# Kernel tuning notes

Hardware: AMD Instinct MI355X
Metric: run time of the kernel (lower is better)

Reference implementation:

```python
import jax, jax.numpy as jnp
import numpy as np

B, S, D, H, DFF = 4, 2048, 1024, 16, 4096
HD = D // H  # head_dim = 64


def rmsnorm(x, scale, eps=1e-6):
    var = jnp.mean(jnp.square(x), axis=-1, keepdims=True)
    return x * jax.lax.rsqrt(var + eps) * scale


def setup_inputs() -> dict:
    key = jax.random.key(0)
    ks = jax.random.split(key, 16)
    s = 1.0 / np.sqrt(D)
    inp = {
        "x": jax.random.normal(ks[0], (B, S, D), jnp.float32),
        "wq": jax.random.normal(ks[1], (D, D), jnp.float32) * s,
        "bq": jnp.zeros((D,), jnp.float32),
        "wk": jax.random.normal(ks[2], (D, D), jnp.float32) * s,
        "bk": jnp.zeros((D,), jnp.float32),
        "wv": jax.random.normal(ks[3], (D, D), jnp.float32) * s,
        "bv": jnp.zeros((D,), jnp.float32),
        "wbeta": jax.random.normal(ks[4], (D, H), jnp.float32) * s,
        "bbeta": jnp.zeros((H,), jnp.float32),
        "wo": jax.random.normal(ks[5], (D, D), jnp.float32) * s,
        "bo": jnp.zeros((D,), jnp.float32),
        "w1": jax.random.normal(ks[6], (D, DFF), jnp.float32) * s,
        "b1": jnp.zeros((DFF,), jnp.float32),
        "w2": jax.random.normal(ks[7], (DFF, D), jnp.float32) * (1.0 / np.sqrt(DFF)),
        "b2": jnp.zeros((D,), jnp.float32),
        "ln1_scale": jnp.ones((D,), jnp.float32),
        "ln2_scale": jnp.ones((D,), jnp.float32),
    }
    return inp


def gdn_attention(x, wq, bq, wk, bk, wv, bv, wbeta, bbeta, wo, bo):
    b, s, _ = x.shape
    q = (x @ wq + bq).reshape(b, s, H, HD)
    k = (x @ wk + bk).reshape(b, s, H, HD)
    v = (x @ wv + bv).reshape(b, s, H, HD)
    k = k / (jnp.linalg.norm(k, axis=-1, keepdims=True) + 1e-6)
    beta = jax.nn.sigmoid(x @ wbeta + bbeta)[..., None]  # (b, s, H, 1)

    # time-major for scan: (s, b, H, ...)
    q = jnp.transpose(q, (1, 0, 2, 3))
    k = jnp.transpose(k, (1, 0, 2, 3))
    v = jnp.transpose(v, (1, 0, 2, 3))
    beta = jnp.transpose(beta, (1, 0, 2, 3))

    def _step(Sm, inputs):
        q_t, k_t, v_t, beta_t = inputs
        Sk = jnp.einsum('bhde,bhe->bhd', Sm, k_t)
        delta = v_t - Sk
        Sm = Sm + beta_t[..., None] * jnp.einsum('bhd,bhe->bhde', delta, k_t)
        o_t = jnp.einsum('bhde,bhe->bhd', Sm, q_t)
        return Sm, o_t

    S0 = jnp.zeros((b, H, HD, HD), x.dtype)
    _, outputs = jax.lax.scan(_step, S0, (q, k, v, beta))
    outputs = jnp.transpose(outputs, (1, 0, 2, 3)).reshape(b, s, D)
    return outputs @ wo + bo


def reference(x, wq, bq, wk, bk, wv, bv, wbeta, bbeta, wo, bo,
              w1, b1, w2, b2, ln1_scale, ln2_scale):
    residual = x
    h = rmsnorm(x, ln1_scale)
    h = gdn_attention(h, wq, bq, wk, bk, wv, bv, wbeta, bbeta, wo, bo)
    x = h + residual
    residual = x
    h = rmsnorm(x, ln2_scale)
    h = jax.nn.gelu(h @ w1 + b1) @ w2 + b2
    return h + residual
```

## Files before the change

kernel.cpp:

```cpp
#include <hip/hip_runtime.h>

#define DEV __device__ __forceinline__

typedef short bf16x8 __attribute__((ext_vector_type(8)));
typedef float f32x4 __attribute__((ext_vector_type(4)));
typedef unsigned int uint;

#define SBAR()   asm volatile("s_barrier" ::: "memory")
#define WAITV(n) asm volatile("s_waitcnt vmcnt(" #n ")" ::: "memory")
#define WAITL()  asm volatile("s_waitcnt lgkmcnt(0)" ::: "memory")

DEV unsigned short f2b(float f) {
    uint u = __float_as_uint(f);
    u += 0x7fffu + ((u >> 16) & 1u);
    return (unsigned short)(u >> 16);
}
DEV uint packbf2(float a, float b) { return (uint)f2b(a) | ((uint)f2b(b) << 16); }
DEV float b2f(unsigned short s) { return __uint_as_float(((uint)s) << 16); }
DEV float b2f_lo(uint u) { return __uint_as_float(u << 16); }
DEV float b2f_hi(uint u) { return __uint_as_float(u & 0xffff0000u); }

DEV void async_cp16(const void* g, void* l) {
    __builtin_amdgcn_global_load_lds(
        (const __attribute__((address_space(1))) unsigned int*)g,
        (__attribute__((address_space(3))) unsigned int*)l, 16, 0, 0);
}

DEV float quad_sum(float x) {
    x += __int_as_float(__builtin_amdgcn_update_dpp(0, __float_as_int(x), 0xB1, 0xF, 0xF, true));
    x += __int_as_float(__builtin_amdgcn_update_dpp(0, __float_as_int(x), 0x4E, 0xF, 0xF, true));
    return x;
}

DEV float gelu_f(float u) {
    float p = u + 0.044715f * u * u * u;
    float e = __expf(-1.5957691216f * p);
    return __fdividef(u, 1.f + e);
}

DEV void dec8(uint4 p, float* o) {
    o[0] = b2f_lo(p.x); o[1] = b2f_hi(p.x); o[2] = b2f_lo(p.y); o[3] = b2f_hi(p.y);
    o[4] = b2f_lo(p.z); o[5] = b2f_hi(p.z); o[6] = b2f_lo(p.w); o[7] = b2f_hi(p.w);
}

__global__ __launch_bounds__(256) void transpose_cast_k(
    const float* __restrict__ in, unsigned short* __restrict__ out, int K, int N)
{
    __shared__ float tile[32][33];
    const int k0 = blockIdx.x * 32, n0 = blockIdx.y * 32;
    const int tx = threadIdx.x & 31, ty = threadIdx.x >> 5;
#pragma unroll
    for (int i = 0; i < 32; i += 8) {
        int n = n0 + tx;
        tile[ty + i][tx] = (n < N) ? in[(size_t)(k0 + ty + i) * N + n] : 0.0f;
    }
    __syncthreads();
#pragma unroll
    for (int i = 0; i < 32; i += 8) {
        out[(size_t)(n0 + ty + i) * K + (k0 + tx)] = f2b(tile[tx][ty + i]);
    }
}

__global__ void build_bias_k(const float* __restrict__ bq, const float* __restrict__ bk,
                             const float* __restrict__ bv, const float* __restrict__ bb,
                             float* __restrict__ outb)
{
    int i = blockIdx.x * 256 + threadIdx.x;
    if (i >= 3328) return;
    float v = 0.f;
    if (i < 1024)      v = bq[i];
    else if (i < 2048) v = bk[i - 1024];
    else if (i < 3072) v = bv[i - 2048];
    else if (i < 3088) v = bb[i - 3072];
    outb[i] = v;
}

__global__ __launch_bounds__(256) void rmsnorm_cast_k(
    const float* __restrict__ x, const float* __restrict__ scale,
    unsigned short* __restrict__ out)
{
    const int row = blockIdx.x;
    const int t = threadIdx.x;
    const float4 v = *(const float4*)(x + (size_t)row * 1024 + t * 4);
    float ss = v.x * v.x + v.y * v.y + v.z * v.z + v.w * v.w;
#pragma unroll
    for (int off = 1; off < 64; off <<= 1) ss += __shfl_xor(ss, off);
    __shared__ float wsum[4];
    if ((t & 63) == 0) wsum[t >> 6] = ss;
    __syncthreads();
    const float tot = wsum[0] + wsum[1] + wsum[2] + wsum[3];
    const float inv = rsqrtf(tot * (1.0f / 1024.0f) + 1e-6f);
    const float4 sc = *(const float4*)(scale + t * 4);
    uint lo = (uint)f2b(v.x * inv * sc.x) | ((uint)f2b(v.y * inv * sc.y) << 16);
    uint hi = (uint)f2b(v.z * inv * sc.z) | ((uint)f2b(v.w * inv * sc.w) << 16);
    uint2 pkd; pkd.x = lo; pkd.y = hi;
    *(uint2*)(out + (size_t)row * 1024 + t * 4) = pkd;
}

template <bool GELU, bool GUARD>
__global__ __launch_bounds__(512, 2) void gemm256(
    const unsigned short* __restrict__ A, const unsigned short* __restrict__ BT,
    const float* __restrict__ bias, unsigned short* __restrict__ C,
    int Nstride, int Nreal, int K)
{
    __shared__ __align__(16) unsigned short As[4][256 * 32];
    __shared__ __align__(16) unsigned short Bs[4][256 * 32];
    const int tid = threadIdx.x;
    const int wid = tid >> 6;
    const int lane = tid & 63;
    const int l16 = lane & 15, quad = lane >> 4;
    const int wm = wid & 1, wn = wid >> 1;
    const int m0 = blockIdx.x << 8, n0 = blockIdx.y << 8;

    const int srow = (wid << 5) + (lane >> 2);
    const int scol = ((lane & 3) ^ ((lane >> 3) & 3)) << 3;
    const unsigned short* Ag = A + (size_t)(m0 + srow) * K + scol;
    const unsigned short* Bg = BT + (size_t)(n0 + srow) * K + scol;
    const size_t rstep16 = (size_t)16 * K;
    const int ldst = wid << 10;

    f32x4 acc[8][4];
#pragma unroll
    for (int i = 0; i < 8; i++)
#pragma unroll
        for (int j = 0; j < 4; j++) acc[i][j] = (f32x4)0.f;

    const int ksw = (quad ^ ((l16 >> 1) & 3)) << 3;
    const int aoff = ((wm << 7) + l16) * 32 + ksw;
    const int boff = ((wn << 6) + l16) * 32 + ksw;

    const int nt = K >> 5;
    async_cp16(Ag, &As[0][ldst]);
    async_cp16(Ag + rstep16, &As[0][ldst + 512]);
    async_cp16(Bg, &Bs[0][ldst]);
    async_cp16(Bg + rstep16, &Bs[0][ldst + 512]);
    async_cp16(Ag + 32, &As[1][ldst]);
    async_cp16(Ag + 32 + rstep16, &As[1][ldst + 512]);
    async_cp16(Bg + 32, &Bs[1][ldst]);
    async_cp16(Bg + 32 + rstep16, &Bs[1][ldst + 512]);
    WAITV(4);
    SBAR();

    for (int tb = 0; tb < nt; tb += 4) {
#pragma unroll
        for (int u = 0; u < 4; ++u) {
            const int t = tb + u;
            const int pb = (u + 2) & 3;
            const bool st = (t + 2) < nt;
            const size_t kpre = (size_t)(t + 2) << 5;
            bf16x8 af[4], bfr[4];
#pragma unroll
            for (int mi = 0; mi < 4; mi++) af[mi] = *(const bf16x8*)&As[u][aoff + mi * 512];
#pragma unroll
            for (int ni = 0; ni < 4; ni++) bfr[ni] = *(const bf16x8*)&Bs[u][boff + ni * 512];
            if (st) {
                async_cp16(Ag + kpre, &As[pb][ldst]);
                async_cp16(Ag + kpre + rstep16, &As[pb][ldst + 512]);
            }
            SBAR();
            WAITL();
            __builtin_amdgcn_s_setprio(1);
#pragma unroll
            for (int mi = 0; mi < 4; mi++)
#pragma unroll
                for (int ni = 0; ni < 4; ni++)
                    acc[mi][ni] = __builtin_amdgcn_mfma_f32_16x16x32_bf16(af[mi], bfr[ni], acc[mi][ni], 0, 0, 0);
            __builtin_amdgcn_s_setprio(0);
            SBAR();
#pragma unroll
            for (int mi = 0; mi < 4; mi++) af[mi] = *(const bf16x8*)&As[u][aoff + (mi + 4) * 512];
            if (st) {
                async_cp16(Bg + kpre, &Bs[pb][ldst]);
                async_cp16(Bg + kpre + rstep16, &Bs[pb][ldst + 512]);
                WAITV(4);
            } else {
                WAITV(0);
            }
            SBAR();
            WAITL();
            __builtin_amdgcn_s_setprio(1);
#pragma unroll
            for (int mi = 0; mi < 4; mi++)
#pragma unroll
                for (int ni = 0; ni < 4; ni++)
                    acc[mi + 4][ni] = __builtin_amdgcn_mfma_f32_16x16x32_bf16(af[mi], bfr[ni], acc[mi + 4][ni], 0, 0, 0);
            __builtin_amdgcn_s_setprio(0);
            SBAR();
        }
    }

    float bv[4];
    const int ccol = n0 + (wn << 6) + l16;
#pragma unroll
    for (int ni = 0; ni < 4; ni++) bv[ni] = bias[ccol + ni * 16];
#pragma unroll
    for (int mi = 0; mi < 8; mi++) {
        const int row = m0 + (wm << 7) + mi * 16 + (quad << 2);
#pragma unroll
        for (int r = 0; r < 4; r++) {
            unsigned short* Crow = C + (size_t)(row + r) * Nstride + ccol;
#pragma unroll
            for (int ni = 0; ni < 4; ni++) {
                float v = acc[mi][ni][r] + bv[ni];
                if (GELU) v = gelu_f(v);
                if (!GUARD || (ccol + ni * 16) < Nreal) Crow[ni * 16] = f2b(v);
            }
        }
    }
}

template <bool ADD>
__global__ __launch_bounds__(512, 2) void gemm128n256(
    const unsigned short* __restrict__ A, const unsigned short* __restrict__ BT,
    const float* __restrict__ bias, const float* __restrict__ add,
    float* __restrict__ C, int N, int K)
{
    __shared__ __align__(16) unsigned short As[4][128 * 32];
    __shared__ __align__(16) unsigned short Bs[4][256 * 32];
    const int tid = threadIdx.x;
    const int wid = tid >> 6;
    const int lane = tid & 63;
    const int l16 = lane & 15, quad = lane >> 4;
    const int wm = wid & 1, wn = wid >> 1;
    const int m0 = blockIdx.x << 7, n0 = blockIdx.y << 8;

    const int arow = (wid << 4) + (lane >> 2);
    const int brow = (wid << 5) + (lane >> 2);
    const int scol = ((lane & 3) ^ ((lane >> 3) & 3)) << 3;
    const unsigned short* Ag = A + (size_t)(m0 + arow) * K + scol;
    const unsigned short* Bg = BT + (size_t)(n0 + brow) * K + scol;
    const size_t rstep16 = (size_t)16 * K;
    const int lda = wid << 9;
    const int ldb = wid << 10;

    f32x4 acc[4][4];
#pragma unroll
    for (int i = 0; i < 4; i++)
#pragma unroll
        for (int j = 0; j < 4; j++) acc[i][j] = (f32x4)0.f;

    const int ksw = (quad ^ ((l16 >> 1) & 3)) << 3;
    const int aoff = ((wm << 6) + l16) * 32 + ksw;
    const int boff = ((wn << 6) + l16) * 32 + ksw;

    const int nt = K >> 5;
    async_cp16(Ag, &As[0][lda]);
    async_cp16(Bg, &Bs[0][ldb]);
    async_cp16(Bg + rstep16, &Bs[0][ldb + 512]);
    async_cp16(Ag + 32, &As[1][lda]);
    async_cp16(Bg + 32, &Bs[1][ldb]);
    async_cp16(Bg + 32 + rstep16, &Bs[1][ldb + 512]);
    WAITV(3);
    SBAR();

    for (int tb = 0; tb < nt; tb += 4) {
#pragma unroll
        for (int u = 0; u < 4; ++u) {
            const int t = tb + u;
            const int pb = (u + 2) & 3;
            const bool st = (t + 2) < nt;
            const size_t kpre = (size_t)(t + 2) << 5;
            bf16x8 af[4], bfr[4];
#pragma unroll
            for (int mi = 0; mi < 4; mi++) af[mi] = *(const bf16x8*)&As[u][aoff + mi * 512];
#pragma unroll
            for (int ni = 0; ni < 4; ni++) bfr[ni] = *(const bf16x8*)&Bs[u][boff + ni * 512];
            if (st) {
                async_cp16(Ag + kpre, &As[pb][lda]);
                async_cp16(Bg + kpre, &Bs[pb][ldb]);
                async_cp16(Bg + kpre + rstep16, &Bs[pb][ldb + 512]);
            }
            SBAR();
            WAITL();
            __builtin_amdgcn_s_setprio(1);
#pragma unroll
            for (int mi = 0; mi < 4; mi++)
#pragma unroll
                for (int ni = 0; ni < 4; ni++)
                    acc[mi][ni] = __builtin_amdgcn_mfma_f32_16x16x32_bf16(af[mi], bfr[ni], acc[mi][ni], 0, 0, 0);
            __builtin_amdgcn_s_setprio(0);
            if (st) { WAITV(3); } else { WAITV(0); }
            SBAR();
        }
    }

    const int ccol = n0 + (wn << 6) + l16;
    float bv[4];
#pragma unroll
    for (int ni = 0; ni < 4; ni++) bv[ni] = bias[ccol + ni * 16];
#pragma unroll
    for (int mi = 0; mi < 4; mi++) {
        const int row = m0 + (wm << 6) + mi * 16 + (quad << 2);
#pragma unroll
        for (int r = 0; r < 4; r++) {
#pragma unroll
            for (int ni = 0; ni < 4; ni++) {
                size_t idx = (size_t)(row + r) * N + ccol + ni * 16;
                float v = acc[mi][ni][r] + bv[ni];
                if (ADD) v += add[idx];
                C[idx] = v;
            }
        }
    }
}


__global__ __launch_bounds__(256) void gdn_prep(
    unsigned short* __restrict__ qkv, unsigned short* __restrict__ Wg,
    unsigned short* __restrict__ ZTg, unsigned short* __restrict__ KTg)
{
    const int chunk = blockIdx.x, bh = blockIdx.y;
    const int b = bh >> 4, h = bh & 15;
    __shared__ float Ks[64 * 68];
    __shared__ float Ws[64 * 65];
    __shared__ float Zs[64 * 65];
    __shared__ float Asl[64 * 65];
    __shared__ float bs[64];
    const int tid = threadIdx.x;
    const int t = tid >> 2, c = tid & 3;
    unsigned short* rowp = qkv + (size_t)(b * 2048 + chunk * 64 + t) * 3200;

    float kn[16];
    {
        uint4 ka = *(const uint4*)(rowp + 1024 + h * 64 + 16 * c);
        uint4 kb = *(const uint4*)(rowp + 1024 + h * 64 + 16 * c + 8);
        dec8(ka, kn); dec8(kb, kn + 8);
    }
    float ss = 0.f;
#pragma unroll
    for (int j = 0; j < 16; j++) ss += kn[j] * kn[j];
    ss = quad_sum(ss);
    const float inv = 1.f / (sqrtf(ss) + 1e-6f);
#pragma unroll
    for (int j = 0; j < 16; j++) kn[j] *= inv;
#pragma unroll
    for (int j = 0; j < 16; j++) Ks[t * 68 + 16 * c + j] = kn[j];
    {
        uint4 p0, p1;
        p0.x = packbf2(kn[0], kn[1]);  p0.y = packbf2(kn[2], kn[3]);
        p0.z = packbf2(kn[4], kn[5]);  p0.w = packbf2(kn[6], kn[7]);
        p1.x = packbf2(kn[8], kn[9]);  p1.y = packbf2(kn[10], kn[11]);
        p1.z = packbf2(kn[12], kn[13]); p1.w = packbf2(kn[14], kn[15]);
        *(uint4*)(rowp + 1024 + h * 64 + 16 * c) = p0;
        *(uint4*)(rowp + 1024 + h * 64 + 16 * c + 8) = p1;
    }
    if (c == 0) bs[t] = 1.f / (1.f + __expf(-b2f(rowp[3072 + h])));
    __syncthreads();

    const float beta = bs[t];
#pragma unroll
    for (int j = 0; j < 16; j++) Ws[t * 65 + 16 * c + j] = beta * kn[j];
    {
        float vv[16];
        uint4 va = *(const uint4*)(rowp + 2048 + h * 64 + 16 * c);
        uint4 vb = *(const uint4*)(rowp + 2048 + h * 64 + 16 * c + 8);
        dec8(va, vv); dec8(vb, vv + 8);
#pragma unroll
        for (int j = 0; j < 16; j++) Zs[t * 65 + 16 * c + j] = beta * vv[j];
    }
    __syncthreads();

    {
        const int tt = tid >> 4, sx = tid & 15;
        float dm[4][4];
#pragma unroll
        for (int i = 0; i < 4; i++)
#pragma unroll
            for (int j = 0; j < 4; j++) dm[i][j] = 0.f;
        for (int d = 0; d < 64; d++) {
            float kt[4], ksv[4];
#pragma unroll
            for (int i = 0; i < 4; i++) kt[i] = Ks[(4 * tt + i) * 68 + d];
#pragma unroll
            for (int j = 0; j < 4; j++) ksv[j] = Ks[(4 * sx + j) * 68 + d];
#pragma unroll
            for (int i = 0; i < 4; i++)
#pragma unroll
                for (int j = 0; j < 4; j++) dm[i][j] += kt[i] * ksv[j];
        }
#pragma unroll
        for (int i = 0; i < 4; i++)
#pragma unroll
            for (int j = 0; j < 4; j++) {
                int T = 4 * tt + i, S_ = 4 * sx + j;
                Asl[T * 65 + S_] = (S_ < T) ? bs[T] * dm[i][j] : 0.f;
            }
    }
    __syncthreads();

    {
        const int wid = tid >> 6, lane = tid & 63;
        for (int qi = 0; qi < 4; qi++) {
            if (qi > 0) {
                const int tb = qi * 16 + wid * 4;
                float aw[4], az[4];
#pragma unroll
                for (int i = 0; i < 4; i++) { aw[i] = Ws[(tb + i) * 65 + lane]; az[i] = Zs[(tb + i) * 65 + lane]; }
                for (int s = 0; s < qi * 16; s++) {
                    float wsv = Ws[s * 65 + lane], zsv = Zs[s * 65 + lane];
#pragma unroll
                    for (int i = 0; i < 4; i++) {
                        float a = Asl[(tb + i) * 65 + s];
                        aw[i] -= a * wsv; az[i] -= a * zsv;
                    }
                }
#pragma unroll
                for (int i = 0; i < 4; i++) { Ws[(tb + i) * 65 + lane] = aw[i]; Zs[(tb + i) * 65 + lane] = az[i]; }
            }
            __syncthreads();
            if (wid == 0) {
                for (int T = qi * 16; T < qi * 16 + 16; T++) {
                    float a_ = Ws[T * 65 + lane];
                    for (int s = qi * 16; s < T; s++) a_ -= Asl[T * 65 + s] * Ws[s * 65 + lane];
                    Ws[T * 65 + lane] = a_;
                }
            } else if (wid == 1) {
                for (int T = qi * 16; T < qi * 16 + 16; T++) {
                    float a_ = Zs[T * 65 + lane];
                    for (int s = qi * 16; s < T; s++) a_ -= Asl[T * 65 + s] * Zs[s * 65 + lane];
                    Zs[T * 65 + lane] = a_;
                }
            }
            __syncthreads();
        }
    }

    const size_t cbase = ((size_t)bh * 32 + chunk) * 4096;
    {
#pragma unroll
        for (int half = 0; half < 2; half++) {
            uint4 w4;
            w4.x = packbf2(Ws[t * 65 + 16 * c + half * 8 + 0], Ws[t * 65 + 16 * c + half * 8 + 1]);
            w4.y = packbf2(Ws[t * 65 + 16 * c + half * 8 + 2], Ws[t * 65 + 16 * c + half * 8 + 3]);
            w4.z = packbf2(Ws[t * 65 + 16 * c + half * 8 + 4], Ws[t * 65 + 16 * c + half * 8 + 5]);
            w4.w = packbf2(Ws[t * 65 + 16 * c + half * 8 + 6], Ws[t * 65 + 16 * c + half * 8 + 7]);
            *(uint4*)(Wg + cbase + (size_t)((2 * c + half) * 64 + t) * 8) = w4;
        }
    }
    {
        const int jj = tid >> 2, tq = tid & 3;
#pragma unroll
        for (int half = 0; half < 2; half++) {
            uint4 z4;
            int i0 = half * 8;
            z4.x = packbf2(Zs[(16 * tq + i0 + 0) * 65 + jj], Zs[(16 * tq + i0 + 1) * 65 + jj]);
            z4.y = packbf2(Zs[(16 * tq + i0 + 2) * 65 + jj], Zs[(16 * tq + i0 + 3) * 65 + jj]);
            z4.z = packbf2(Zs[(16 * tq + i0 + 4) * 65 + jj], Zs[(16 * tq + i0 + 5) * 65 + jj]);
            z4.w = packbf2(Zs[(16 * tq + i0 + 6) * 65 + jj], Zs[(16 * tq + i0 + 7) * 65 + jj]);
            *(uint4*)(ZTg + cbase + (size_t)((2 * tq + half) * 64 + jj) * 8) = z4;
        }
    }
    {
        const int dd = tid >> 2, tq = tid & 3;
#pragma unroll
        for (int half = 0; half < 2; half++) {
            uint4 k4;
            int i0 = half * 8;
            k4.x = packbf2(Ks[(16 * tq + i0 + 0) * 68 + dd], Ks[(16 * tq + i0 + 1) * 68 + dd]);
            k4.y = packbf2(Ks[(16 * tq + i0 + 2) * 68 + dd], Ks[(16 * tq + i0 + 3) * 68 + dd]);
            k4.z = packbf2(Ks[(16 * tq + i0 + 4) * 68 + dd], Ks[(16 * tq + i0 + 5) * 68 + dd]);
            k4.w = packbf2(Ks[(16 * tq + i0 + 6) * 68 + dd], Ks[(16 * tq + i0 + 7) * 68 + dd]);
            *(uint4*)(KTg + cbase + (size_t)((2 * tq + half) * 64 + dd) * 8) = k4;
        }
    }
}

__global__ __launch_bounds__(256, 1) void gdn_prop_mfma(
    const unsigned short* __restrict__ Wg, const unsigned short* __restrict__ KTg,
    const unsigned short* __restrict__ ZTg, unsigned short* __restrict__ Sg,
    unsigned short* __restrict__ YTg)
{
    const int bh = blockIdx.x;
    __shared__ unsigned short WbU[4096];
    __shared__ unsigned short KTbU[4096];
    __shared__ unsigned short ZTbU[4096];
    __shared__ unsigned short SbU[4096];
    const int tid = threadIdx.x;
    const int wid = tid >> 6;
    const int lane = tid & 63;
    const int l16 = lane & 15, quad = lane >> 4;

    f32x4 Sacc[4];
#pragma unroll
    for (int dt = 0; dt < 4; dt++) Sacc[dt] = (f32x4)0.f;

    for (int ch = 0; ch < 32; ch++) {
        const size_t cbase = ((size_t)bh * 32 + ch) * 4096;
#pragma unroll
        for (int p = 0; p < 2; p++) {
            const int n = wid * 2 + p;
            async_cp16(Wg + cbase + n * 512 + lane * 8, &WbU[n * 512]);
            async_cp16(KTg + cbase + n * 512 + lane * 8, &KTbU[n * 512]);
            async_cp16(ZTg + cbase + n * 512 + lane * 8, &ZTbU[n * 512]);
        }
#pragma unroll
        for (int dt = 0; dt < 4; dt++) {
#pragma unroll
            for (int r = 0; r < 4; r++) {
                const int j = wid * 16 + quad * 4 + r;
                SbU[((2 * dt + (l16 >> 3)) * 64 + j) * 8 + (l16 & 7)] = f2b(Sacc[dt][r]);
            }
        }
        __syncthreads();

        {
            uint4 sa0 = *(const uint4*)&SbU[tid * 16];
            uint4 sa1 = *(const uint4*)&SbU[tid * 16 + 8];
            *(uint4*)(Sg + cbase + tid * 16) = sa0;
            *(uint4*)(Sg + cbase + tid * 16 + 8) = sa1;
        }

        f32x4 t1[4];
#pragma unroll
        for (int tt = 0; tt < 4; tt++) t1[tt] = (f32x4)0.f;
#pragma unroll
        for (int kh = 0; kh < 2; kh++) {
            const int g = kh * 4 + quad;
            bf16x8 afr = *(const bf16x8*)&SbU[(g * 64 + wid * 16 + l16) * 8];
#pragma unroll
            for (int tt = 0; tt < 4; tt++) {
                bf16x8 bfr = *(const bf16x8*)&WbU[(g * 64 + tt * 16 + l16) * 8];
                t1[tt] = __builtin_amdgcn_mfma_f32_16x16x32_bf16(afr, bfr, t1[tt], 0, 0, 0);
            }
        }
#pragma unroll
        for (int tt = 0; tt < 4; tt++) {
            const int t = tt * 16 + l16;
            const int gb = (t >> 3) * 64;
            unsigned short ybf[4];
#pragma unroll
            for (int r = 0; r < 4; r++) {
                const int j = wid * 16 + quad * 4 + r;
                const float z = b2f(ZTbU[(gb + j) * 8 + (t & 7)]);
                ybf[r] = f2b(z - t1[tt][r]);
            }
#pragma unroll
            for (int r = 0; r < 4; r++) {
                const int j = wid * 16 + quad * 4 + r;
                ZTbU[(gb + j) * 8 + (t & 7)] = ybf[r];
            }
        }
#pragma unroll
        for (int kh = 0; kh < 2; kh++) {
            const int g = kh * 4 + quad;
            bf16x8 afr = *(const bf16x8*)&ZTbU[(g * 64 + wid * 16 + l16) * 8];
#pragma unroll
            for (int dt = 0; dt < 4; dt++) {
                bf16x8 bfr = *(const bf16x8*)&KTbU[(g * 64 + dt * 16 + l16) * 8];
                Sacc[dt] = __builtin_amdgcn_mfma_f32_16x16x32_bf16(afr, bfr, Sacc[dt], 0, 0, 0);
            }
        }
#pragma unroll
        for (int pp = 0; pp < 2; pp++) {
            const int p = lane * 2 + pp;
            const int g = p >> 4, jj = p & 15;
            const int off = (g * 64 + wid * 16 + jj) * 8;
            uint4 yv = *(const uint4*)&ZTbU[off];
            *(uint4*)(YTg + cbase + off) = yv;
        }
        __syncthreads();
    }
}

__global__ __launch_bounds__(256) void gdn_out(
    const unsigned short* __restrict__ qkv, const unsigned short* __restrict__ YTg,
    const unsigned short* __restrict__ Sg, unsigned short* __restrict__ attn)
{
    const int chunk = blockIdx.x, bh = blockIdx.y;
    const int b = bh >> 4, h = bh & 15;
    __shared__ unsigned short QbU[8 * 516];
    __shared__ unsigned short KbU[8 * 516];
    __shared__ unsigned short StU[8 * 516];
    __shared__ unsigned short YtU[8 * 516];
    __shared__ unsigned short MhU[8 * 516];
    __shared__ unsigned short MlU[8 * 516];
    const int tid = threadIdx.x;
    const int wid = tid >> 6, lane = tid & 63;
    const int l16 = lane & 15, quad = lane >> 4;
    const size_t cbase = ((size_t)bh * 32 + chunk) * 4096;

    {
        const int t = tid >> 2, c = tid & 3;
        const unsigned short* rowp = qkv + (size_t)(b * 2048 + chunk * 64 + t) * 3200;
        uint4 qa = *(const uint4*)(rowp + h * 64 + 16 * c);
        uint4 qb = *(const uint4*)(rowp + h * 64 + 16 * c + 8);
        uint4 ka = *(const uint4*)(rowp + 1024 + h * 64 + 16 * c);
        uint4 kb = *(const uint4*)(rowp + 1024 + h * 64 + 16 * c + 8);
        *(uint4*)&QbU[(2 * c) * 516 + t * 8]     = qa;
        *(uint4*)&QbU[(2 * c + 1) * 516 + t * 8] = qb;
        *(uint4*)&KbU[(2 * c) * 516 + t * 8]     = ka;
        *(uint4*)&KbU[(2 * c + 1) * 516 + t * 8] = kb;
        const int g = tid >> 5, row = (tid * 2) & 63;
        uint4 s0 = *(const uint4*)(Sg + cbase + tid * 16);
        uint4 s1 = *(const uint4*)(Sg + cbase + tid * 16 + 8);
        *(uint4*)&StU[g * 516 + row * 8]       = s0;
        *(uint4*)&StU[g * 516 + (row + 1) * 8] = s1;
        uint4 y0 = *(const uint4*)(YTg + cbase + tid * 16);
        uint4 y1 = *(const uint4*)(YTg + cbase + tid * 16 + 8);
        *(uint4*)&YtU[g * 516 + row * 8]       = y0;
        *(uint4*)&YtU[g * 516 + (row + 1) * 8] = y1;
    }
    __syncthreads();

    f32x4 m[4], o[4];
#pragma unroll
    for (int i = 0; i < 4; i++) { m[i] = (f32x4)0.f; o[i] = (f32x4)0.f; }

#pragma unroll
    for (int kh = 0; kh < 2; kh++) {
        const int g = kh * 4 + quad;
        bf16x8 afr = *(const bf16x8*)&QbU[g * 516 + (wid * 16 + l16) * 8];
#pragma unroll
        for (int st = 0; st < 4; st++) {
            bf16x8 bk = *(const bf16x8*)&KbU[g * 516 + (st * 16 + l16) * 8];
            m[st] = __builtin_amdgcn_mfma_f32_16x16x32_bf16(afr, bk, m[st], 0, 0, 0);
        }
#pragma unroll
        for (int jt = 0; jt < 4; jt++) {
            bf16x8 bs_ = *(const bf16x8*)&StU[g * 516 + (jt * 16 + l16) * 8];
            o[jt] = __builtin_amdgcn_mfma_f32_16x16x32_bf16(afr, bs_, o[jt], 0, 0, 0);
        }
    }

#pragma unroll
    for (int st = 0; st < 4; st++) {
#pragma unroll
        for (int r = 0; r < 4; r++) {
            const int t = wid * 16 + quad * 4 + r;
            const int s = st * 16 + l16;
            float v = (s <= t) ? m[st][r] : 0.f;
            unsigned short hi = f2b(v);
            unsigned short lo = f2b(v - b2f(hi));
            const int addr = (s >> 3) * 516 + t * 8 + (s & 7);
            MhU[addr] = hi;
            MlU[addr] = lo;
        }
    }
    __syncthreads();

#pragma unroll
    for (int kh = 0; kh < 2; kh++) {
        const int g = kh * 4 + quad;
        bf16x8 ah = *(const bf16x8*)&MhU[g * 516 + (wid * 16 + l16) * 8];
        bf16x8 al = *(const bf16x8*)&MlU[g * 516 + (wid * 16 + l16) * 8];
#pragma unroll
        for (int jt = 0; jt < 4; jt++) {
            bf16x8 by = *(const bf16x8*)&YtU[g * 516 + (jt * 16 + l16) * 8];
            o[jt] = __builtin_amdgcn_mfma_f32_16x16x32_bf16(ah, by, o[jt], 0, 0, 0);
            o[jt] = __builtin_amdgcn_mfma_f32_16x16x32_bf16(al, by, o[jt], 0, 0, 0);
        }
    }

#pragma unroll
    for (int jt = 0; jt < 4; jt++) {
#pragma unroll
        for (int r = 0; r < 4; r++) {
            const int t = wid * 16 + quad * 4 + r;
            attn[(size_t)(b * 2048 + chunk * 64 + t) * 1024 + h * 64 + jt * 16 + l16] = f2b(o[jt][r]);
        }
    }
}

static constexpr size_t OFF_H     = 0;
static constexpr size_t OFF_WQKVT = OFF_H + 16777216;
static constexpr size_t OFF_WOT   = OFF_WQKVT + 6553600;
static constexpr size_t OFF_W1T   = OFF_WOT + 2097152;
static constexpr size_t OFF_W2T   = OFF_W1T + 8388608;
static constexpr size_t OFF_BIAS  = OFF_W2T + 8388608;
static constexpr size_t OFF_QKV   = OFF_BIAS + 16384;
static constexpr size_t OFF_ATTN  = OFF_QKV + 67108864;
static constexpr size_t OFF_Y1    = OFF_ATTN + 16777216;
static constexpr size_t OFF_WG    = OFF_Y1 + 33554432;
static constexpr size_t OFF_YG    = OFF_WG + 16777216;

extern "C" void kernel_launch(void* const* d_in, const int* in_sizes, int n_in,
                              void* d_out, int out_size, void* d_ws, size_t ws_size,
                              hipStream_t stream)
{
    const float* x     = (const float*)d_in[0];
    const float* wq    = (const float*)d_in[1];
    const float* bq    = (const float*)d_in[2];
    const float* wk    = (const float*)d_in[3];
    const float* bk    = (const float*)d_in[4];
    const float* wv    = (const float*)d_in[5];
    const float* bv    = (const float*)d_in[6];
    const float* wbeta = (const float*)d_in[7];
    const float* bbeta = (const float*)d_in[8];
    const float* wo    = (const float*)d_in[9];
    const float* bo    = (const float*)d_in[10];
    const float* w1    = (const float*)d_in[11];
    const float* b1    = (const float*)d_in[12];
    const float* w2    = (const float*)d_in[13];
    const float* b2    = (const float*)d_in[14];
    const float* ln1   = (const float*)d_in[15];
    const float* ln2   = (const float*)d_in[16];

    char* ws = (char*)d_ws;
    unsigned short* hbuf  = (unsigned short*)(ws + OFF_H);
    unsigned short* Sg    = (unsigned short*)(ws + OFF_H);
    unsigned short* wqkvT = (unsigned short*)(ws + OFF_WG);
    unsigned short* woT   = (unsigned short*)(ws + OFF_WOT);
    unsigned short* w1T   = (unsigned short*)(ws + OFF_W1T);
    unsigned short* w2T   = (unsigned short*)(ws + OFF_W2T);
    float*          biasc = (float*)(ws + OFF_BIAS);
    unsigned short* qkvU  = (unsigned short*)(ws + OFF_QKV);
    unsigned short* gbuf  = (unsigned short*)(ws + OFF_QKV);
    unsigned short* attn  = (unsigned short*)(ws + OFF_ATTN);
    float*          y1    = (float*)(ws + OFF_Y1);
    unsigned short* ZTg   = (unsigned short*)(ws + OFF_Y1);
    unsigned short* KTg   = (unsigned short*)(ws + OFF_Y1 + 16777216);
    unsigned short* Wg    = (unsigned short*)(ws + OFF_WG);
    unsigned short* YTg   = (unsigned short*)(ws + OFF_YG);
    float*          out   = (float*)d_out;

    transpose_cast_k<<<dim3(32, 32), 256, 0, stream>>>(wq, wqkvT,               1024, 1024);
    transpose_cast_k<<<dim3(32, 32), 256, 0, stream>>>(wk, wqkvT + 1024 * 1024, 1024, 1024);
    transpose_cast_k<<<dim3(32, 32), 256, 0, stream>>>(wv, wqkvT + 2048 * 1024, 1024, 1024);
    transpose_cast_k<<<dim3(32, 8),  256, 0, stream>>>(wbeta, wqkvT + 3072 * 1024, 1024, 16);
    transpose_cast_k<<<dim3(32, 32), 256, 0, stream>>>(wo, woT, 1024, 1024);
    transpose_cast_k<<<dim3(32, 128), 256, 0, stream>>>(w1, w1T, 1024, 4096);
    transpose_cast_k<<<dim3(128, 32), 256, 0, stream>>>(w2, w2T, 4096, 1024);
    build_bias_k<<<13, 256, 0, stream>>>(bq, bk, bv, bbeta, biasc);

    rmsnorm_cast_k<<<8192, 256, 0, stream>>>(x, ln1, hbuf);
    gemm256<false, true><<<dim3(32, 13), 512, 0, stream>>>(hbuf, wqkvT, biasc, qkvU, 3200, 3200, 1024);
    gdn_prep<<<dim3(32, 64), 256, 0, stream>>>(qkvU, Wg, ZTg, KTg);
    gdn_prop_mfma<<<64, 256, 0, stream>>>(Wg, KTg, ZTg, Sg, YTg);
    gdn_out<<<dim3(32, 64), 256, 0, stream>>>(qkvU, YTg, Sg, attn);
    gemm128n256<true><<<dim3(64, 4), 512, 0, stream>>>(attn, woT, bo, x, y1, 1024, 1024);
    rmsnorm_cast_k<<<8192, 256, 0, stream>>>(y1, ln2, hbuf);
    gemm256<true, false><<<dim3(32, 16), 512, 0, stream>>>(hbuf, w1T, b1, gbuf, 4096, 4096, 1024);
    gemm128n256<true><<<dim3(64, 4), 512, 0, stream>>>(gbuf, w2T, b2, y1, out, 1024, 4096);
}
```

Before: 626.7 us.

## Double-buffer GDN chunk propagation loads and simplify GEMM main-loop barrier schedule

The sequential per-head gdn_prop_mfma kernel now double-buffers the W, KT and ZT chunk tiles in LDS, prefetching chunk ch+1 while chunk ch is processed. The intent is to hide global load latency on the serial 32-chunk recurrence, which runs one block per (batch, head). In the large GEMM, the two half-step MFMA phases are merged into a single phase: all 8 A fragments are loaded at once, which removes a barrier pair but raises register pressure. The smaller GEMM moves its vmcnt wait before the MFMAs, and explicit lgkmcnt waits are dropped there, which relies on the compiler inserting waits for the LDS reads.

```diff
diff --git a/kernel.cpp b/kernel.cpp
--- a/kernel.cpp
+++ b/kernel.cpp
@@ -148,28 +148,14 @@
             const int pb = (u + 2) & 3;
             const bool st = (t + 2) < nt;
             const size_t kpre = (size_t)(t + 2) << 5;
-            bf16x8 af[4], bfr[4];
-#pragma unroll
-            for (int mi = 0; mi < 4; mi++) af[mi] = *(const bf16x8*)&As[u][aoff + mi * 512];
+            bf16x8 af[8], bfr[4];
+#pragma unroll
+            for (int mi = 0; mi < 8; mi++) af[mi] = *(const bf16x8*)&As[u][aoff + mi * 512];
 #pragma unroll
             for (int ni = 0; ni < 4; ni++) bfr[ni] = *(const bf16x8*)&Bs[u][boff + ni * 512];
             if (st) {
                 async_cp16(Ag + kpre, &As[pb][ldst]);
                 async_cp16(Ag + kpre + rstep16, &As[pb][ldst + 512]);
-            }
-            SBAR();
-            WAITL();
-            __builtin_amdgcn_s_setprio(1);
-#pragma unroll
-            for (int mi = 0; mi < 4; mi++)
-#pragma unroll
-                for (int ni = 0; ni < 4; ni++)
-                    acc[mi][ni] = __builtin_amdgcn_mfma_f32_16x16x32_bf16(af[mi], bfr[ni], acc[mi][ni], 0, 0, 0);
-            __builtin_amdgcn_s_setprio(0);
-            SBAR();
-#pragma unroll
-            for (int mi = 0; mi < 4; mi++) af[mi] = *(const bf16x8*)&As[u][aoff + (mi + 4) * 512];
-            if (st) {
                 async_cp16(Bg + kpre, &Bs[pb][ldst]);
                 async_cp16(Bg + kpre + rstep16, &Bs[pb][ldst + 512]);
                 WAITV(4);
@@ -177,13 +163,12 @@
                 WAITV(0);
             }
             SBAR();
-            WAITL();
             __builtin_amdgcn_s_setprio(1);
 #pragma unroll
-            for (int mi = 0; mi < 4; mi++)
+            for (int mi = 0; mi < 8; mi++)
 #pragma unroll
                 for (int ni = 0; ni < 4; ni++)
-                    acc[mi + 4][ni] = __builtin_amdgcn_mfma_f32_16x16x32_bf16(af[mi], bfr[ni], acc[mi + 4][ni], 0, 0, 0);
+                    acc[mi][ni] = __builtin_amdgcn_mfma_f32_16x16x32_bf16(af[mi], bfr[ni], acc[mi][ni], 0, 0, 0);
             __builtin_amdgcn_s_setprio(0);
             SBAR();
         }
@@ -269,9 +254,11 @@
                 async_cp16(Ag + kpre, &As[pb][lda]);
                 async_cp16(Bg + kpre, &Bs[pb][ldb]);
                 async_cp16(Bg + kpre + rstep16, &Bs[pb][ldb + 512]);
+                WAITV(3);
+            } else {
+                WAITV(0);
             }
             SBAR();
-            WAITL();
             __builtin_amdgcn_s_setprio(1);
 #pragma unroll
             for (int mi = 0; mi < 4; mi++)
@@ -279,7 +266,6 @@
                 for (int ni = 0; ni < 4; ni++)
                     acc[mi][ni] = __builtin_amdgcn_mfma_f32_16x16x32_bf16(af[mi], bfr[ni], acc[mi][ni], 0, 0, 0);
             __builtin_amdgcn_s_setprio(0);
-            if (st) { WAITV(3); } else { WAITV(0); }
             SBAR();
         }
     }
@@ -471,9 +457,9 @@
     unsigned short* __restrict__ YTg)
 {
     const int bh = blockIdx.x;
-    __shared__ unsigned short WbU[4096];
-    __shared__ unsigned short KTbU[4096];
-    __shared__ unsigned short ZTbU[4096];
+    __shared__ unsigned short WbU[2][4096];
+    __shared__ unsigned short KTbU[2][4096];
+    __shared__ unsigned short ZTbU[2][4096];
     __shared__ unsigned short SbU[4096];
     const int tid = threadIdx.x;
     const int wid = tid >> 6;
@@ -484,14 +470,35 @@
 #pragma unroll
     for (int dt = 0; dt < 4; dt++) Sacc[dt] = (f32x4)0.f;
 
-    for (int ch = 0; ch < 32; ch++) {
-        const size_t cbase = ((size_t)bh * 32 + ch) * 4096;
+    {
+        const size_t cb0 = ((size_t)bh * 32) * 4096;
 #pragma unroll
         for (int p = 0; p < 2; p++) {
             const int n = wid * 2 + p;
-            async_cp16(Wg + cbase + n * 512 + lane * 8, &WbU[n * 512]);
-            async_cp16(KTg + cbase + n * 512 + lane * 8, &KTbU[n * 512]);
-            async_cp16(ZTg + cbase + n * 512 + lane * 8, &ZTbU[n * 512]);
+            async_cp16(Wg + cb0 + n * 512 + lane * 8, &WbU[0][n * 512]);
+            async_cp16(KTg + cb0 + n * 512 + lane * 8, &KTbU[0][n * 512]);
+            async_cp16(ZTg + cb0 + n * 512 + lane * 8, &ZTbU[0][n * 512]);
+        }
+    }
+    WAITV(0);
+    SBAR();
+
+    for (int ch = 0; ch < 32; ch++) {
+        const int cur = ch & 1, nxt = cur ^ 1;
+        const size_t cbase = ((size_t)bh * 32 + ch) * 4096;
+        unsigned short* Wb  = WbU[cur];
+        unsigned short* KTb = KTbU[cur];
+        unsigned short* ZTb = ZTbU[cur];
+
+        if (ch + 1 < 32) {
+            const size_t cbn = cbase + 4096;
+#pragma unroll
+            for (int p = 0; p < 2; p++) {
+                const int n = wid * 2 + p;
+                async_cp16(Wg + cbn + n * 512 + lane * 8, &WbU[nxt][n * 512]);
+                async_cp16(KTg + cbn + n * 512 + lane * 8, &KTbU[nxt][n * 512]);
+                async_cp16(ZTg + cbn + n * 512 + lane * 8, &ZTbU[nxt][n * 512]);
+            }
         }
 #pragma unroll
         for (int dt = 0; dt < 4; dt++) {
@@ -501,7 +508,8 @@
                 SbU[((2 * dt + (l16 >> 3)) * 64 + j) * 8 + (l16 & 7)] = f2b(Sacc[dt][r]);
             }
         }
-        __syncthreads();
+        WAITL();
+        SBAR();
 
         {
             uint4 sa0 = *(const uint4*)&SbU[tid * 16];
@@ -519,7 +527,7 @@
             bf16x8 afr = *(const bf16x8*)&SbU[(g * 64 + wid * 16 + l16) * 8];
 #pragma unroll
             for (int tt = 0; tt < 4; tt++) {
-                bf16x8 bfr = *(const bf16x8*)&WbU[(g * 64 + tt * 16 + l16) * 8];
+                bf16x8 bfr = *(const bf16x8*)&Wb[(g * 64 + tt * 16 + l16) * 8];
                 t1[tt] = __builtin_amdgcn_mfma_f32_16x16x32_bf16(afr, bfr, t1[tt], 0, 0, 0);
             }
         }
@@ -531,22 +539,22 @@
 #pragma unroll
             for (int r = 0; r < 4; r++) {
                 const int j = wid * 16 + quad * 4 + r;
-                const float z = b2f(ZTbU[(gb + j) * 8 + (t & 7)]);
+                const float z = b2f(ZTb[(gb + j) * 8 + (t & 7)]);
                 ybf[r] = f2b(z - t1[tt][r]);
             }
 #pragma unroll
             for (int r = 0; r < 4; r++) {
                 const int j = wid * 16 + quad * 4 + r;
-                ZTbU[(gb + j) * 8 + (t & 7)] = ybf[r];
+                ZTb[(gb + j) * 8 + (t & 7)] = ybf[r];
             }
         }
 #pragma unroll
         for (int kh = 0; kh < 2; kh++) {
             const int g = kh * 4 + quad;
-            bf16x8 afr = *(const bf16x8*)&ZTbU[(g * 64 + wid * 16 + l16) * 8];
+            bf16x8 afr = *(const bf16x8*)&ZTb[(g * 64 + wid * 16 + l16) * 8];
 #pragma unroll
             for (int dt = 0; dt < 4; dt++) {
-                bf16x8 bfr = *(const bf16x8*)&KTbU[(g * 64 + dt * 16 + l16) * 8];
+                bf16x8 bfr = *(const bf16x8*)&KTb[(g * 64 + dt * 16 + l16) * 8];
                 Sacc[dt] = __builtin_amdgcn_mfma_f32_16x16x32_bf16(afr, bfr, Sacc[dt], 0, 0, 0);
             }
         }
@@ -555,10 +563,11 @@
             const int p = lane * 2 + pp;
             const int g = p >> 4, jj = p & 15;
             const int off = (g * 64 + wid * 16 + jj) * 8;
-            uint4 yv = *(const uint4*)&ZTbU[off];
+            uint4 yv = *(const uint4*)&ZTb[off];
             *(uint4*)(YTg + cbase + off) = yv;
         }
-        __syncthreads();
+        WAITV(0);
+        SBAR();
     }
 }
 
```

Result: faster. 596.1 us (-4.9%).
